# Optimization experiments

Hardware: AMD Instinct MI355X
Metric: run time of the kernel (lower is better)

The kernel has to match this reference:

```python
import jax, jax.numpy as jnp
import numpy as np

S, B, C = 7, 2, 20
E = B * 5 + C  # 30
BATCH = 16384


def setup_inputs() -> dict:
    key = jax.random.key(0)
    k1, k2, k3 = jax.random.split(key, 3)
    # keep coords in [0.05, 0.95) so sqrt(w,h) stays well-defined (original would NaN on negatives)
    pred = 0.05 + 0.9 * jax.random.uniform(k1, (BATCH, S, S, E), dtype=jnp.float32)
    tgt = 0.05 + 0.9 * jax.random.uniform(k2, (BATCH, S, S, E), dtype=jnp.float32)
    conf = (jax.random.uniform(k3, (BATCH, S, S)) < 0.3).astype(jnp.float32)
    # both per-cell boxes carry the same objectness target (channels 4 and 9), exactly 0 or 1
    tgt = tgt.at[..., 4].set(conf).at[..., 9].set(conf)
    return {"pred_tensor": pred, "target_tensor": tgt}


def _iou_vs_first(pb, t0):
    # pb: [..., B, 4], t0: [..., 4]; boxes treated as raw corners [x1,y1,x2,y2]
    # (faithful to original compute_iou which does NOT convert xywh -> corners)
    t = t0[..., None, :]  # [..., 1, 4]
    lt = jnp.maximum(pb[..., :2], t[..., :2])
    rb = jnp.minimum(pb[..., 2:4], t[..., 2:4])
    wh = jnp.maximum(rb - lt, 0.0)
    inter = wh[..., 0] * wh[..., 1]                            # [..., B]
    a1 = (pb[..., 2] - pb[..., 0]) * (pb[..., 3] - pb[..., 1])  # [..., B]
    a2 = (t[..., 2] - t[..., 0]) * (t[..., 3] - t[..., 1])      # [..., 1]
    return inter / (a1 + a2 - inter)


def reference(pred_tensor, target_tensor):
    dt = pred_tensor.dtype
    m = (target_tensor[..., 4] > 0).astype(dt)    # obj cell mask  [N,S,S]
    nm = (target_tensor[..., 4] == 0).astype(dt)  # noobj cell mask [N,S,S]

    lead = pred_tensor.shape[:3]
    pb = pred_tensor[..., : B * 5].reshape(*lead, B, 5)    # [N,S,S,B,5]
    tb = target_tensor[..., : B * 5].reshape(*lead, B, 5)  # [N,S,S,B,5]

    # IoU of each predicted box vs the FIRST target box of the cell (box_target[i] in the loop)
    iou = _iou_vs_first(pb[..., :4], tb[..., 0, :4])  # [N,S,S,B]
    max_iou = jnp.max(iou, axis=-1)                   # [N,S,S]
    resp = jax.nn.one_hot(jnp.argmax(iou, axis=-1), B, dtype=dt)  # responsible-box mask [N,S,S,B]
    w = m[..., None] * resp                           # per-box responsibility weight

    loss_xy = jnp.sum(w * jnp.sum((pb[..., :2] - tb[..., :2]) ** 2, axis=-1))
    loss_wh = jnp.sum(w * jnp.sum((jnp.sqrt(pb[..., 2:4]) - jnp.sqrt(tb[..., 2:4])) ** 2, axis=-1))
    # original stores max_iou via .data -> detached target
    loss_obj = jnp.sum(w * (pb[..., 4] - jax.lax.stop_gradient(max_iou)[..., None]) ** 2)
    loss_noobj = jnp.sum(nm * ((pred_tensor[..., 4] - target_tensor[..., 4]) ** 2
                               + (pred_tensor[..., 9] - target_tensor[..., 9]) ** 2))
    loss_class = jnp.sum(m[..., None] * (pred_tensor[..., B * 5:] - target_tensor[..., B * 5:]) ** 2)
    return (loss_xy, loss_wh, loss_obj, loss_noobj, loss_class)
```

## Files before the change

kernel.cpp:

```cpp
#include <hip/hip_runtime.h>

constexpr int S = 7, NB = 2, C = 20, E = 30;
constexpr int BATCH = 16384;
constexpr int NCELLS = BATCH * S * S;

__global__ void zero_out_kernel(float* out) {
    if (threadIdx.x < 5) out[threadIdx.x] = 0.0f;
}

__global__ __launch_bounds__(256, 4) void yolo_loss_kernel(
    const float* __restrict__ pred,
    const float* __restrict__ tgt,
    float* __restrict__ out)
{
    const int tid      = blockIdx.x * blockDim.x + threadIdx.x;
    const int nthreads = gridDim.x * blockDim.x;
    const int lane     = threadIdx.x & 63;
    const int wv       = threadIdx.x >> 6;

    float acc0 = 0.f, acc1 = 0.f, acc2 = 0.f, acc3 = 0.f, acc4 = 0.f;

    for (int cell = tid; cell < NCELLS; cell += nthreads) {
        const float2* gp = reinterpret_cast<const float2*>(pred) + (size_t)cell * 15;
        const float2* gt = reinterpret_cast<const float2*>(tgt)  + (size_t)cell * 15;

        float p[30], t[30];
        #pragma unroll
        for (int j = 0; j < 15; ++j) {
            float2 a = gp[j]; p[2*j] = a.x; p[2*j+1] = a.y;
        }
        #pragma unroll
        for (int j = 0; j < 15; ++j) {
            float2 b = gt[j]; t[2*j] = b.x; t[2*j+1] = b.y;
        }

        const float tconf = t[4];
        const float m  = (tconf > 0.0f)  ? 1.0f : 0.0f;
        const float nm = 1.0f - m;

        const float t0x1 = t[0], t0y1 = t[1], t0x2 = t[2], t0y2 = t[3];
        const float a2 = (t0x2 - t0x1) * (t0y2 - t0y1);

        float iou0, iou1;
        {
            const float ltx = fmaxf(p[0], t0x1), lty = fmaxf(p[1], t0y1);
            const float rbx = fminf(p[2], t0x2), rby = fminf(p[3], t0y2);
            const float wx = fmaxf(rbx - ltx, 0.0f), wy = fmaxf(rby - lty, 0.0f);
            const float inter = wx * wy;
            const float a1 = (p[2] - p[0]) * (p[3] - p[1]);
            iou0 = inter / (a1 + a2 - inter);
        }
        {
            const float ltx = fmaxf(p[5], t0x1), lty = fmaxf(p[6], t0y1);
            const float rbx = fminf(p[7], t0x2), rby = fminf(p[8], t0y2);
            const float wx = fmaxf(rbx - ltx, 0.0f), wy = fmaxf(rby - lty, 0.0f);
            const float inter = wx * wy;
            const float a1 = (p[7] - p[5]) * (p[8] - p[6]);
            iou1 = inter / (a1 + a2 - inter);
        }

        const float max_iou = fmaxf(iou0, iou1);
        const bool b1 = iou1 > iou0;

        const float rpx = b1 ? p[5] : p[0];
        const float rpy = b1 ? p[6] : p[1];
        const float rpw = b1 ? p[7] : p[2];
        const float rph = b1 ? p[8] : p[3];
        const float rpc = b1 ? p[9] : p[4];
        const float rtx = b1 ? t[5] : t[0];
        const float rty = b1 ? t[6] : t[1];
        const float rtw = b1 ? t[7] : t[2];
        const float rth = b1 ? t[8] : t[3];

        {
            const float dx = rpx - rtx;
            const float dy = rpy - rty;
            acc0 += m * (dx*dx + dy*dy);
        }
        {
            const float dw = sqrtf(rpw) - sqrtf(rtw);
            const float dh = sqrtf(rph) - sqrtf(rth);
            acc1 += m * (dw*dw + dh*dh);
        }
        {
            const float d = rpc - max_iou;
            acc2 += m * d * d;
        }
        {
            const float d0 = p[4] - t[4];
            const float d1 = p[9] - t[9];
            acc3 += nm * (d0*d0 + d1*d1);
        }
        {
            float cl = 0.f;
            #pragma unroll
            for (int k = 10; k < 30; ++k) {
                const float d = p[k] - t[k];
                cl += d * d;
            }
            acc4 += m * cl;
        }
    }

    float acc[5] = {acc0, acc1, acc2, acc3, acc4};
    __shared__ float wave_sums[4][5];
    #pragma unroll
    for (int i = 0; i < 5; ++i) {
        float v = acc[i];
        #pragma unroll
        for (int o = 32; o > 0; o >>= 1)
            v += __shfl_down(v, o, 64);
        if (lane == 0) wave_sums[wv][i] = v;
    }
    __syncthreads();

    if (threadIdx.x < 5) {
        const float v = wave_sums[0][threadIdx.x] + wave_sums[1][threadIdx.x]
                      + wave_sums[2][threadIdx.x] + wave_sums[3][threadIdx.x];
        atomicAdd(out + threadIdx.x, v);
    }
}

extern "C" void kernel_launch(void* const* d_in, const int* in_sizes, int n_in,
                              void* d_out, int out_size, void* d_ws, size_t ws_size,
                              hipStream_t stream) {
    const float* pred = (const float*)d_in[0];
    const float* tgt  = (const float*)d_in[1];
    float* out = (float*)d_out;

    hipLaunchKernelGGL(zero_out_kernel, dim3(1), dim3(64), 0, stream, out);

    hipLaunchKernelGGL(yolo_loss_kernel, dim3(1024), dim3(256), 0, stream,
                       pred, tgt, out);
}
```

Measured before the change: 218.8 us.

## Stage cell tiles into LDS via async global_load_lds with double buffering

```diff
diff --git a/kernel.cpp b/kernel.cpp
--- a/kernel.cpp
+++ b/kernel.cpp
@@ -1,41 +1,79 @@
 #include <hip/hip_runtime.h>
+#include <stdint.h>
 
-constexpr int S = 7, NB = 2, C = 20, E = 30;
-constexpr int BATCH = 16384;
-constexpr int NCELLS = BATCH * S * S;
+constexpr int NCELLS = 802816;
+constexpr int TILE   = 64;
+constexpr int NTILES = NCELLS / TILE;
+constexpr int NWAVES = 1280;
+constexpr int TBYTES = TILE * 30 * 4;
 
 __global__ void zero_out_kernel(float* out) {
     if (threadIdx.x < 5) out[threadIdx.x] = 0.0f;
 }
 
-__global__ __launch_bounds__(256, 4) void yolo_loss_kernel(
+typedef const uint32_t __attribute__((address_space(1)))* gptr_t;
+typedef uint32_t       __attribute__((address_space(3)))* lptr_t;
+
+__global__ __launch_bounds__(64, 1) void yolo_loss_kernel(
     const float* __restrict__ pred,
     const float* __restrict__ tgt,
     float* __restrict__ out)
 {
-    const int tid      = blockIdx.x * blockDim.x + threadIdx.x;
-    const int nthreads = gridDim.x * blockDim.x;
-    const int lane     = threadIdx.x & 63;
-    const int wv       = threadIdx.x >> 6;
+    __shared__ float smem[2][2 * TBYTES / 4];
+    const int lane = threadIdx.x;
 
     float acc0 = 0.f, acc1 = 0.f, acc2 = 0.f, acc3 = 0.f, acc4 = 0.f;
 
-    for (int cell = tid; cell < NCELLS; cell += nthreads) {
-        const float2* gp = reinterpret_cast<const float2*>(pred) + (size_t)cell * 15;
-        const float2* gt = reinterpret_cast<const float2*>(tgt)  + (size_t)cell * 15;
+    char* const bufA = (char*)&smem[0][0];
+    char* const bufB = (char*)&smem[1][0];
 
+#define STAGE(DST, TI)                                                        \
+    {                                                                         \
+        const char* gsp = (const char*)pred + (size_t)(TI) * TBYTES;          \
+        const char* gst = (const char*)tgt  + (size_t)(TI) * TBYTES;          \
+        _Pragma("unroll")                                                     \
+        for (int j = 0; j < 7; ++j) {                                         \
+            __builtin_amdgcn_global_load_lds(                                 \
+                (gptr_t)(gsp + j * 1024 + lane * 16),                         \
+                (lptr_t)(void*)((DST) + j * 1024), 16, 0, 0);                 \
+            __builtin_amdgcn_global_load_lds(                                 \
+                (gptr_t)(gst + j * 1024 + lane * 16),                         \
+                (lptr_t)(void*)((DST) + TBYTES + j * 1024), 16, 0, 0);        \
+        }                                                                     \
+        _Pragma("unroll")                                                     \
+        for (int j = 0; j < 2; ++j) {                                         \
+            __builtin_amdgcn_global_load_lds(                                 \
+                (gptr_t)(gsp + 7168 + j * 256 + lane * 4),                    \
+                (lptr_t)(void*)((DST) + 7168 + j * 256), 4, 0, 0);            \
+            __builtin_amdgcn_global_load_lds(                                 \
+                (gptr_t)(gst + 7168 + j * 256 + lane * 4),                    \
+                (lptr_t)(void*)((DST) + TBYTES + 7168 + j * 256), 4, 0, 0);   \
+        }                                                                     \
+    }
+
+    int tile = blockIdx.x;
+    char* cur = bufA;
+    char* nxt = bufB;
+    STAGE(cur, tile);
+
+    for (; tile < NTILES; tile += NWAVES) {
+        int ntile = tile + NWAVES;
+        if (ntile >= NTILES) ntile = tile;
+        STAGE(nxt, ntile);
+        asm volatile("s_waitcnt vmcnt(18)" ::: "memory");
+        __builtin_amdgcn_sched_barrier(0);
+
+        const float2* myp = (const float2*)(cur)          + lane * 15;
+        const float2* myt = (const float2*)(cur + TBYTES) + lane * 15;
         float p[30], t[30];
         #pragma unroll
         for (int j = 0; j < 15; ++j) {
-            float2 a = gp[j]; p[2*j] = a.x; p[2*j+1] = a.y;
-        }
-        #pragma unroll
-        for (int j = 0; j < 15; ++j) {
-            float2 b = gt[j]; t[2*j] = b.x; t[2*j+1] = b.y;
+            float2 a = myp[j]; p[2*j] = a.x; p[2*j+1] = a.y;
+            float2 b = myt[j]; t[2*j] = b.x; t[2*j+1] = b.y;
         }
 
         const float tconf = t[4];
-        const float m  = (tconf > 0.0f)  ? 1.0f : 0.0f;
+        const float m  = (tconf > 0.0f) ? 1.0f : 0.0f;
         const float nm = 1.0f - m;
 
         const float t0x1 = t[0], t0y1 = t[1], t0x2 = t[2], t0y2 = t[3];
@@ -73,8 +111,7 @@
         const float rth = b1 ? t[8] : t[3];
 
         {
-            const float dx = rpx - rtx;
-            const float dy = rpy - rty;
+            const float dx = rpx - rtx, dy = rpy - rty;
             acc0 += m * (dx*dx + dy*dy);
         }
         {
@@ -100,24 +137,21 @@
             }
             acc4 += m * cl;
         }
+
+        { char* tmp = cur; cur = nxt; nxt = tmp; }
     }
+#undef STAGE
+
+    asm volatile("s_waitcnt vmcnt(0)" ::: "memory");
 
     float acc[5] = {acc0, acc1, acc2, acc3, acc4};
-    __shared__ float wave_sums[4][5];
     #pragma unroll
     for (int i = 0; i < 5; ++i) {
         float v = acc[i];
         #pragma unroll
         for (int o = 32; o > 0; o >>= 1)
             v += __shfl_down(v, o, 64);
-        if (lane == 0) wave_sums[wv][i] = v;
-    }
-    __syncthreads();
-
-    if (threadIdx.x < 5) {
-        const float v = wave_sums[0][threadIdx.x] + wave_sums[1][threadIdx.x]
-                      + wave_sums[2][threadIdx.x] + wave_sums[3][threadIdx.x];
-        atomicAdd(out + threadIdx.x, v);
+        if (lane == 0) atomicAdd(out + i, v);
     }
 }
 
@@ -130,6 +164,6 @@
 
     hipLaunchKernelGGL(zero_out_kernel, dim3(1), dim3(64), 0, stream, out);
 
-    hipLaunchKernelGGL(yolo_loss_kernel, dim3(1024), dim3(256), 0, stream,
+    hipLaunchKernelGGL(yolo_loss_kernel, dim3(NWAVES), dim3(64), 0, stream,
                        pred, tgt, out);
 }
```

Measured after the change: 275.5 us. 1.26x slower.
